# Kernel optimization log

Measured on AMD Instinct MI355X. Metric: run time of the kernel, lower is better.

The kernel has to match this reference:

```python
import jax, jax.numpy as jnp
import numpy as np

# CrossAttention (DFFNet): 1x1 convs produce q,k from depth and v from rgb;
# full dense attention over hw spatial tokens: softmax(q^T k) then v @ mask^T.

def setup_inputs() -> dict:
    key = jax.random.key(0)
    ks = jax.random.split(key, 8)
    B, C, H, W = 4, 256, 64, 64
    Cqk = C // 8  # ratio=8 -> 32
    s = 0.02
    return {
        "rgb":   jax.random.normal(ks[0], (B, C, H, W), jnp.float32),
        "depth": jax.random.normal(ks[1], (B, C, H, W), jnp.float32),
        "Wq": jax.random.normal(ks[2], (Cqk, C), jnp.float32) * s,
        "bq": jax.random.normal(ks[3], (Cqk,), jnp.float32) * s,
        "Wk": jax.random.normal(ks[4], (Cqk, C), jnp.float32) * s,
        "bk": jax.random.normal(ks[5], (Cqk,), jnp.float32) * s,
        "Wv": jax.random.normal(ks[6], (C, C), jnp.float32) * s,
        "bv": jax.random.normal(ks[7], (C,), jnp.float32) * s,
    }


def reference(rgb, depth, Wq, bq, Wk, bk, Wv, bv):
    B, C, H, W = rgb.shape
    hw = H * W
    d = depth.reshape(B, C, hw)   # [B, C, hw]
    r = rgb.reshape(B, C, hw)     # [B, C, hw]
    # 1x1 convs == channel-mixing linear maps
    q = jnp.einsum('oc,bcn->bon', Wq, d) + bq[None, :, None]  # [B, Cqk, hw]
    k = jnp.einsum('oc,bcn->bon', Wk, d) + bk[None, :, None]  # [B, Cqk, hw]
    v = jnp.einsum('oc,bcn->bon', Wv, r) + bv[None, :, None]  # [B, C, hw]
    # scores: q^T k -> [B, hw, hw], softmax over last dim
    scores = jnp.einsum('bcn,bcm->bnm', q, k)
    mask = jax.nn.softmax(scores, axis=-1)
    # feat = v @ mask^T  -> [B, C, hw]
    feat = jnp.einsum('bcm,bnm->bcn', v, mask)
    return feat.reshape(B, C, H, W)
```

## Files before the change

kernel.cpp:

```cpp
#include <hip/hip_runtime.h>
#include <stdint.h>

#define L2E 1.44269504088896340736f

typedef _Float16 half8 __attribute__((ext_vector_type(8)));
typedef float floatx4 __attribute__((ext_vector_type(4)));

static __device__ __forceinline__ unsigned short f32_to_f16u(float f) {
  union { _Float16 h; unsigned short s; } cv; cv.h = (_Float16)f; return cv.s;
}

__global__ __launch_bounds__(256) void proj_kernel(
    const float* __restrict__ rgb,
    const float* __restrict__ depth,
    const float* __restrict__ Wq, const float* __restrict__ bq,
    const float* __restrict__ Wk, const float* __restrict__ bk,
    const float* __restrict__ Wv, const float* __restrict__ bv,
    unsigned short* __restrict__ qT,
    unsigned short* __restrict__ kT,
    unsigned short* __restrict__ v)
{
  __shared__ __align__(16) unsigned short sW[64 * 256];

  const int n0 = blockIdx.x * 64;
  const int b  = blockIdx.y;
  const int z  = blockIdx.z;
  const int t  = threadIdx.x;
  const int w  = t >> 6;
  const int lane = t & 63;
  const int l15 = lane & 15;
  const int q4  = lane >> 4;

  const float* X = (z == 0) ? depth : rgb;
  const float* xb = X + (size_t)b * 256 * 4096;
  const int n_row = n0 + 16 * w + l15;
  const int colbase = (z == 0) ? 0 : (z - 1) * 64;

#pragma unroll
  for (int it = 0; it < 8; it++) {
    int L = it * 256 + t;
    int og = L >> 5;
    int phys = L & 31;
    int ci = phys ^ (og & 7);
    const float* wr;
    if (z == 0) wr = (og < 32) ? (Wq + (size_t)og * 256) : (Wk + (size_t)(og - 32) * 256);
    else        wr = Wv + (size_t)(colbase + og) * 256;
    float4 w0 = *(const float4*)(wr + ci * 8);
    float4 w1 = *(const float4*)(wr + ci * 8 + 4);
    half8 h;
    h[0] = (_Float16)w0.x; h[1] = (_Float16)w0.y; h[2] = (_Float16)w0.z; h[3] = (_Float16)w0.w;
    h[4] = (_Float16)w1.x; h[5] = (_Float16)w1.y; h[6] = (_Float16)w1.z; h[7] = (_Float16)w1.w;
    *(half8*)&sW[(size_t)L * 8] = h;
  }

  float bias[4];
#pragma unroll
  for (int ct = 0; ct < 4; ct++) {
    int og = ct * 16 + l15;
    if (z == 0) bias[ct] = (og < 32) ? bq[og] : bk[og - 32];
    else        bias[ct] = bv[colbase + og];
  }
  __syncthreads();

  floatx4 acc[4];
#pragma unroll
  for (int i = 0; i < 4; i++) acc[i] = (floatx4){0.f, 0.f, 0.f, 0.f};

#pragma unroll
  for (int ks = 0; ks < 8; ks++) {
    const int c0 = ks * 32;
    half8 a;
#pragma unroll
    for (int j = 0; j < 8; j++) {
      int c = c0 + q4 * 8 + j;
      a[j] = (_Float16)xb[(size_t)c * 4096 + n_row];
    }
    const int ci = ks * 4 + q4;
#pragma unroll
    for (int ct = 0; ct < 4; ct++) {
      int og = ct * 16 + l15;
      half8 bf = *(const half8*)&sW[og * 256 + ((ci ^ (og & 7)) * 8)];
      acc[ct] = __builtin_amdgcn_mfma_f32_16x16x32_f16(a, bf, acc[ct], 0, 0, 0);
    }
  }

  __syncthreads();

  if (z == 0) {
#pragma unroll
    for (int ct = 0; ct < 4; ct++) {
      int og = ct * 16 + l15;
#pragma unroll
      for (int r = 0; r < 4; r++) {
        int n = n0 + 16 * w + q4 * 4 + r;
        unsigned short hv = f32_to_f16u(acc[ct][r] + bias[ct]);
        if (og < 32) qT[((size_t)b * 4096 + n) * 32 + og] = hv;
        else         kT[((size_t)b * 4096 + n) * 32 + (og - 32)] = hv;
      }
    }
  } else {
    unsigned short* tile = sW;
#pragma unroll
    for (int ct = 0; ct < 4; ct++) {
#pragma unroll
      for (int r = 0; r < 4; r++) {
        int co_l = ct * 16 + l15;
        int nl = 16 * w + q4 * 4 + r;
        tile[co_l * 72 + nl] = f32_to_f16u(acc[ct][r] + bias[ct]);
      }
    }
    __syncthreads();
#pragma unroll
    for (int it = 0; it < 2; it++) {
      int co_l = it * 32 + (t >> 3);
      int ch = t & 7;
      int4 val = *(const int4*)&tile[co_l * 72 + ch * 8];
      *(int4*)&v[((size_t)b * 256 + colbase + co_l) * 4096 + n0 + ch * 8] = val;
    }
  }
}

__global__ __launch_bounds__(256, 4) void attn_kernel(
    const unsigned short* __restrict__ qT,
    const unsigned short* __restrict__ kT,
    const unsigned short* __restrict__ v,
    unsigned short* __restrict__ Op,
    float* __restrict__ lW)
{
  __shared__ __align__(16) unsigned char smem[36864];
  unsigned short* sV = (unsigned short*)smem;
  unsigned short* sK = (unsigned short*)(smem + 16384);
  unsigned short* sP = (unsigned short*)(smem + 18432);

  const int n0 = blockIdx.x * 64;
  const int b  = blockIdx.y;
  const int chunk = blockIdx.z;
  const int t  = threadIdx.x;
  const int w  = t >> 6;
  const int lane = t & 63;
  const int l15 = lane & 15;
  const int q4  = lane >> 4;

  const unsigned short* qrow = qT + ((size_t)b * 4096 + n0 + 16 * w + l15) * 32 + q4 * 8;
  half8 aq = *(const half8*)qrow;

  const unsigned short* vB = v  + (size_t)b * 256 * 4096;
  const unsigned short* kB = kT + (size_t)b * 4096 * 32;
  unsigned short* sPw = sP + w * 640;

  float lsum[4] = {0.f, 0.f, 0.f, 0.f};
  floatx4 acc[16];
#pragma unroll
  for (int ct = 0; ct < 16; ct++) acc[ct] = (floatx4){0.f, 0.f, 0.f, 0.f};
  const floatx4 zf = (floatx4){0.f, 0.f, 0.f, 0.f};

  const int mbase = chunk * 1024;
  for (int mi = 0; mi < 1024; mi += 32) {
    const int m0 = mbase + mi;
    __syncthreads();
#pragma unroll
    for (int j = 0; j < 4; j++) {
      int lin = j * 256 + t;
      int c = lin >> 2;
      int p = lin & 3;
      int lc = p ^ ((c >> 1) & 3);
      uint4 val = *(const uint4*)&vB[(size_t)c * 4096 + m0 + lc * 8];
      *(uint4*)&sV[lin * 8] = val;
    }
    if (t < 128) {
      int m = t >> 2, p = t & 3, lc = p ^ ((m >> 1) & 3);
      uint4 val = *(const uint4*)&kB[(size_t)(m0 + m) * 32 + lc * 8];
      *(uint4*)&sK[t * 8] = val;
    }
    __syncthreads();

    half8 bk0 = *(const half8*)&sK[l15 * 32 + ((q4 ^ ((l15 >> 1) & 3)) * 8)];
    half8 bk1 = *(const half8*)&sK[(16 + l15) * 32 + ((q4 ^ (((16 + l15) >> 1) & 3)) * 8)];
    floatx4 s0 = __builtin_amdgcn_mfma_f32_16x16x32_f16(aq, bk0, zf, 0, 0, 0);
    floatx4 s1 = __builtin_amdgcn_mfma_f32_16x16x32_f16(aq, bk1, zf, 0, 0, 0);

    float p0[4], p1[4];
#pragma unroll
    for (int r = 0; r < 4; r++) {
      p0[r] = exp2f(s0[r] * L2E);
      p1[r] = exp2f(s1[r] * L2E);
      lsum[r] += p0[r] + p1[r];
    }
#pragma unroll
    for (int r = 0; r < 4; r++) {
      int row = q4 * 4 + r;
      sPw[row * 40 + l15]      = f32_to_f16u(p0[r]);
      sPw[row * 40 + 16 + l15] = f32_to_f16u(p1[r]);
    }
    asm volatile("s_waitcnt lgkmcnt(0)" ::: "memory");
    half8 ap = *(const half8*)&sPw[l15 * 40 + q4 * 8];
#pragma unroll
    for (int ct = 0; ct < 16; ct++) {
      int co = ct * 16 + l15;
      half8 bv8 = *(const half8*)&sV[co * 32 + ((q4 ^ ((co >> 1) & 3)) * 8)];
      acc[ct] = __builtin_amdgcn_mfma_f32_16x16x32_f16(ap, bv8, acc[ct], 0, 0, 0);
    }
  }

#pragma unroll
  for (int off = 1; off < 16; off <<= 1) {
#pragma unroll
    for (int r = 0; r < 4; r++) lsum[r] += __shfl_xor(lsum[r], off);
  }
  if (l15 == 0) {
#pragma unroll
    for (int r = 0; r < 4; r++)
      lW[((size_t)chunk * 4 + b) * 4096 + n0 + 16 * w + q4 * 4 + r] = lsum[r];
  }

  unsigned short* sO = (unsigned short*)smem;
#pragma unroll
  for (int pass = 0; pass < 2; pass++) {
    __syncthreads();
#pragma unroll
    for (int cl = 0; cl < 8; cl++) {
      int ct = pass * 8 + cl;
      int co_l = cl * 16 + l15;
#pragma unroll
      for (int r = 0; r < 4; r++) {
        int nl = 16 * w + q4 * 4 + r;
        sO[co_l * 72 + nl] = f32_to_f16u(acc[ct][r]);
      }
    }
    __syncthreads();
#pragma unroll
    for (int s = 0; s < 4; s++) {
      int co_l = s * 32 + (t >> 3);
      int ch = t & 7;
      int4 val = *(const int4*)&sO[co_l * 72 + ch * 8];
      *(int4*)&Op[(((size_t)chunk * 4 + b) * 256 + pass * 128 + co_l) * 4096 + n0 + ch * 8] = val;
    }
  }
}

__global__ __launch_bounds__(256) void combine_kernel(
    const unsigned short* __restrict__ Op,
    const float* __restrict__ lW,
    float* __restrict__ out)
{
  const int t = threadIdx.x;
  const int b = blockIdx.y;
  const size_t n8 = (size_t)blockIdx.x * 2048 + (size_t)t * 8;
  const int co0 = blockIdx.z * 8;

  float sum[8] = {0.f, 0.f, 0.f, 0.f, 0.f, 0.f, 0.f, 0.f};
#pragma unroll
  for (int ch = 0; ch < 4; ch++) {
    const float* lp = lW + ((size_t)ch * 4 + b) * 4096 + n8;
    float4 a0 = *(const float4*)lp;
    float4 a1 = *(const float4*)(lp + 4);
    sum[0] += a0.x; sum[1] += a0.y; sum[2] += a0.z; sum[3] += a0.w;
    sum[4] += a1.x; sum[5] += a1.y; sum[6] += a1.z; sum[7] += a1.w;
  }
  float rl[8];
#pragma unroll
  for (int i = 0; i < 8; i++) rl[i] = 1.0f / sum[i];

#pragma unroll
  for (int cc = 0; cc < 8; cc++) {
    int co = co0 + cc;
    float o[8] = {0.f, 0.f, 0.f, 0.f, 0.f, 0.f, 0.f, 0.f};
#pragma unroll
    for (int ch = 0; ch < 4; ch++) {
      half8 hv = *(const half8*)&Op[(((size_t)ch * 4 + b) * 256 + co) * 4096 + n8];
#pragma unroll
      for (int i = 0; i < 8; i++) o[i] += (float)hv[i];
    }
    float* op = out + ((size_t)b * 256 + co) * 4096 + n8;
    float4 r0, r1;
    r0.x = o[0] * rl[0]; r0.y = o[1] * rl[1]; r0.z = o[2] * rl[2]; r0.w = o[3] * rl[3];
    r1.x = o[4] * rl[4]; r1.y = o[5] * rl[5]; r1.z = o[6] * rl[6]; r1.w = o[7] * rl[7];
    *(float4*)op = r0;
    *(float4*)(op + 4) = r1;
  }
}

extern "C" void kernel_launch(void* const* d_in, const int* in_sizes, int n_in,
                              void* d_out, int out_size, void* d_ws, size_t ws_size,
                              hipStream_t stream) {
  const float* rgb   = (const float*)d_in[0];
  const float* depth = (const float*)d_in[1];
  const float* Wq    = (const float*)d_in[2];
  const float* bq    = (const float*)d_in[3];
  const float* Wk    = (const float*)d_in[4];
  const float* bk    = (const float*)d_in[5];
  const float* Wv    = (const float*)d_in[6];
  const float* bv    = (const float*)d_in[7];
  float* out = (float*)d_out;

  unsigned short* qT = (unsigned short*)d_ws;
  unsigned short* kT = qT + (size_t)4 * 4096 * 32;
  unsigned short* vW = kT + (size_t)4 * 4096 * 32;
  unsigned short* Op = vW + (size_t)4 * 256 * 4096;
  float* lW = (float*)(Op + (size_t)4 * 4 * 256 * 4096);

  dim3 pg(64, 4, 5);
  proj_kernel<<<pg, 256, 0, stream>>>(rgb, depth, Wq, bq, Wk, bk, Wv, bv, qT, kT, vW);
  dim3 ag(64, 4, 4);
  attn_kernel<<<ag, 256, 0, stream>>>(qT, kT, vW, Op, lW);
  dim3 cg(2, 4, 32);
  combine_kernel<<<cg, 256, 0, stream>>>(Op, lW, out);
}
```

Baseline: 172.0 us.

## Split attention channels across blocks and use 32x32 MFMA for PV

The attention kernel now splits the 256 output channels into two halves across blocks, doubling the grid. It switches the P·V product to 32x32x16 MFMA tiles with P shared through LDS by all waves, and loads K directly from global into registers instead of staging it in LDS. Smaller LDS and accumulator footprints allow higher occupancy hints, at the cost of recomputing QK scores and exponentials twice per query tile and adding an extra barrier per iteration. The projection kernel prefetches the next input slice into registers, and the combine kernel is flattened to one channel per block.

Result: slower. 196.5 us (+14.2%).

```diff
diff --git a/kernel.cpp b/kernel.cpp
--- a/kernel.cpp
+++ b/kernel.cpp
@@ -5,12 +5,14 @@
 
 typedef _Float16 half8 __attribute__((ext_vector_type(8)));
 typedef float floatx4 __attribute__((ext_vector_type(4)));
+typedef float floatx16 __attribute__((ext_vector_type(16)));
 
 static __device__ __forceinline__ unsigned short f32_to_f16u(float f) {
   union { _Float16 h; unsigned short s; } cv; cv.h = (_Float16)f; return cv.s;
 }
-
-__global__ __launch_bounds__(256) void proj_kernel(
+static __device__ __forceinline__ _Float16 f32h(float f) { return (_Float16)f; }
+
+__global__ __launch_bounds__(256, 5) void proj_kernel(
     const float* __restrict__ rgb,
     const float* __restrict__ depth,
     const float* __restrict__ Wq, const float* __restrict__ bq,
@@ -30,10 +32,11 @@
   const int lane = t & 63;
   const int l15 = lane & 15;
   const int q4  = lane >> 4;
+  const int n_row = n0 + 16 * w + l15;
 
   const float* X = (z == 0) ? depth : rgb;
   const float* xb = X + (size_t)b * 256 * 4096;
-  const int n_row = n0 + 16 * w + l15;
+  const float* xrow = xb + n_row;
   const int colbase = (z == 0) ? 0 : (z - 1) * 64;
 
 #pragma unroll
@@ -48,8 +51,8 @@
     float4 w0 = *(const float4*)(wr + ci * 8);
     float4 w1 = *(const float4*)(wr + ci * 8 + 4);
     half8 h;
-    h[0] = (_Float16)w0.x; h[1] = (_Float16)w0.y; h[2] = (_Float16)w0.z; h[3] = (_Float16)w0.w;
-    h[4] = (_Float16)w1.x; h[5] = (_Float16)w1.y; h[6] = (_Float16)w1.z; h[7] = (_Float16)w1.w;
+    h[0] = f32h(w0.x); h[1] = f32h(w0.y); h[2] = f32h(w0.z); h[3] = f32h(w0.w);
+    h[4] = f32h(w1.x); h[5] = f32h(w1.y); h[6] = f32h(w1.z); h[7] = f32h(w1.w);
     *(half8*)&sW[(size_t)L * 8] = h;
   }
 
@@ -66,14 +69,19 @@
 #pragma unroll
   for (int i = 0; i < 4; i++) acc[i] = (floatx4){0.f, 0.f, 0.f, 0.f};
 
+  float af[8];
+#pragma unroll
+  for (int j = 0; j < 8; j++) af[j] = xrow[(size_t)(q4 * 8 + j) * 4096];
+
 #pragma unroll
   for (int ks = 0; ks < 8; ks++) {
-    const int c0 = ks * 32;
     half8 a;
 #pragma unroll
-    for (int j = 0; j < 8; j++) {
-      int c = c0 + q4 * 8 + j;
-      a[j] = (_Float16)xb[(size_t)c * 4096 + n_row];
+    for (int j = 0; j < 8; j++) a[j] = (_Float16)af[j];
+    if (ks < 7) {
+#pragma unroll
+      for (int j = 0; j < 8; j++)
+        af[j] = xrow[(size_t)(ks * 32 + 32 + q4 * 8 + j) * 4096];
     }
     const int ci = ks * 4 + q4;
 #pragma unroll
@@ -120,46 +128,53 @@
   }
 }
 
-__global__ __launch_bounds__(256, 4) void attn_kernel(
+__global__ __launch_bounds__(256, 6) void attn_kernel(
     const unsigned short* __restrict__ qT,
     const unsigned short* __restrict__ kT,
     const unsigned short* __restrict__ v,
     unsigned short* __restrict__ Op,
     float* __restrict__ lW)
 {
-  __shared__ __align__(16) unsigned char smem[36864];
+  __shared__ __align__(16) unsigned char smem[18432];
   unsigned short* sV = (unsigned short*)smem;
-  unsigned short* sK = (unsigned short*)(smem + 16384);
-  unsigned short* sP = (unsigned short*)(smem + 18432);
+  unsigned short* sP = (unsigned short*)(smem + 8192);
 
   const int n0 = blockIdx.x * 64;
   const int b  = blockIdx.y;
-  const int chunk = blockIdx.z;
+  const int chunk = blockIdx.z >> 1;
+  const int half  = blockIdx.z & 1;
   const int t  = threadIdx.x;
   const int w  = t >> 6;
   const int lane = t & 63;
   const int l15 = lane & 15;
   const int q4  = lane >> 4;
+  const int l31 = lane & 31;
+  const int hi  = lane >> 5;
+  const int co0 = half * 128;
 
   const unsigned short* qrow = qT + ((size_t)b * 4096 + n0 + 16 * w + l15) * 32 + q4 * 8;
   half8 aq = *(const half8*)qrow;
 
-  const unsigned short* vB = v  + (size_t)b * 256 * 4096;
+  const unsigned short* vB = v  + (size_t)b * 256 * 4096 + (size_t)co0 * 4096;
   const unsigned short* kB = kT + (size_t)b * 4096 * 32;
-  unsigned short* sPw = sP + w * 640;
 
   float lsum[4] = {0.f, 0.f, 0.f, 0.f};
-  floatx4 acc[16];
-#pragma unroll
-  for (int ct = 0; ct < 16; ct++) acc[ct] = (floatx4){0.f, 0.f, 0.f, 0.f};
+  floatx16 acc[2];
+#pragma unroll
+  for (int nt = 0; nt < 2; nt++)
+#pragma unroll
+    for (int i = 0; i < 16; i++) acc[nt][i] = 0.f;
   const floatx4 zf = (floatx4){0.f, 0.f, 0.f, 0.f};
 
   const int mbase = chunk * 1024;
   for (int mi = 0; mi < 1024; mi += 32) {
     const int m0 = mbase + mi;
+    half8 bk0 = *(const half8*)&kB[(size_t)(m0 + l15) * 32 + q4 * 8];
+    half8 bk1 = *(const half8*)&kB[(size_t)(m0 + 16 + l15) * 32 + q4 * 8];
+
     __syncthreads();
 #pragma unroll
-    for (int j = 0; j < 4; j++) {
+    for (int j = 0; j < 2; j++) {
       int lin = j * 256 + t;
       int c = lin >> 2;
       int p = lin & 3;
@@ -167,15 +182,8 @@
       uint4 val = *(const uint4*)&vB[(size_t)c * 4096 + m0 + lc * 8];
       *(uint4*)&sV[lin * 8] = val;
     }
-    if (t < 128) {
-      int m = t >> 2, p = t & 3, lc = p ^ ((m >> 1) & 3);
-      uint4 val = *(const uint4*)&kB[(size_t)(m0 + m) * 32 + lc * 8];
-      *(uint4*)&sK[t * 8] = val;
-    }
     __syncthreads();
 
-    half8 bk0 = *(const half8*)&sK[l15 * 32 + ((q4 ^ ((l15 >> 1) & 3)) * 8)];
-    half8 bk1 = *(const half8*)&sK[(16 + l15) * 32 + ((q4 ^ (((16 + l15) >> 1) & 3)) * 8)];
     floatx4 s0 = __builtin_amdgcn_mfma_f32_16x16x32_f16(aq, bk0, zf, 0, 0, 0);
     floatx4 s1 = __builtin_amdgcn_mfma_f32_16x16x32_f16(aq, bk1, zf, 0, 0, 0);
 
@@ -188,17 +196,22 @@
     }
 #pragma unroll
     for (int r = 0; r < 4; r++) {
-      int row = q4 * 4 + r;
-      sPw[row * 40 + l15]      = f32_to_f16u(p0[r]);
-      sPw[row * 40 + 16 + l15] = f32_to_f16u(p1[r]);
-    }
-    asm volatile("s_waitcnt lgkmcnt(0)" ::: "memory");
-    half8 ap = *(const half8*)&sPw[l15 * 40 + q4 * 8];
-#pragma unroll
-    for (int ct = 0; ct < 16; ct++) {
-      int co = ct * 16 + l15;
-      half8 bv8 = *(const half8*)&sV[co * 32 + ((q4 ^ ((co >> 1) & 3)) * 8)];
-      acc[ct] = __builtin_amdgcn_mfma_f32_16x16x32_f16(ap, bv8, acc[ct], 0, 0, 0);
+      int row = w * 16 + q4 * 4 + r;
+      sP[row * 40 + l15]      = f32_to_f16u(p0[r]);
+      sP[row * 40 + 16 + l15] = f32_to_f16u(p1[r]);
+    }
+    __syncthreads();
+
+    const int c_lw = w * 32 + l31;
+#pragma unroll
+    for (int kst = 0; kst < 2; kst++) {
+      int lc = (kst * 2 + hi) ^ ((c_lw >> 1) & 3);
+      half8 bvv = *(const half8*)&sV[(c_lw * 4 + lc) * 8];
+#pragma unroll
+      for (int nt = 0; nt < 2; nt++) {
+        half8 ap = *(const half8*)&sP[(nt * 32 + l31) * 40 + kst * 16 + hi * 8];
+        acc[nt] = __builtin_amdgcn_mfma_f32_32x32x16_f16(ap, bvv, acc[nt], 0, 0, 0);
+      }
     }
   }
 
@@ -207,34 +220,35 @@
 #pragma unroll
     for (int r = 0; r < 4; r++) lsum[r] += __shfl_xor(lsum[r], off);
   }
-  if (l15 == 0) {
+  if (half == 0 && l15 == 0) {
 #pragma unroll
     for (int r = 0; r < 4; r++)
       lW[((size_t)chunk * 4 + b) * 4096 + n0 + 16 * w + q4 * 4 + r] = lsum[r];
   }
 
+  __syncthreads();
   unsigned short* sO = (unsigned short*)smem;
-#pragma unroll
-  for (int pass = 0; pass < 2; pass++) {
-    __syncthreads();
-#pragma unroll
-    for (int cl = 0; cl < 8; cl++) {
-      int ct = pass * 8 + cl;
-      int co_l = cl * 16 + l15;
-#pragma unroll
-      for (int r = 0; r < 4; r++) {
-        int nl = 16 * w + q4 * 4 + r;
-        sO[co_l * 72 + nl] = f32_to_f16u(acc[ct][r]);
-      }
-    }
-    __syncthreads();
-#pragma unroll
-    for (int s = 0; s < 4; s++) {
-      int co_l = s * 32 + (t >> 3);
-      int ch = t & 7;
-      int4 val = *(const int4*)&sO[co_l * 72 + ch * 8];
-      *(int4*)&Op[(((size_t)chunk * 4 + b) * 256 + pass * 128 + co_l) * 4096 + n0 + ch * 8] = val;
-    }
+  const int co_l = w * 32 + l31;
+#pragma unroll
+  for (int nt = 0; nt < 2; nt++) {
+#pragma unroll
+    for (int g = 0; g < 4; g++) {
+      int nl = nt * 32 + g * 8 + hi * 4;
+      ushort4 pk;
+      pk.x = f32_to_f16u(acc[nt][g * 4 + 0]);
+      pk.y = f32_to_f16u(acc[nt][g * 4 + 1]);
+      pk.z = f32_to_f16u(acc[nt][g * 4 + 2]);
+      pk.w = f32_to_f16u(acc[nt][g * 4 + 3]);
+      *(ushort4*)&sO[co_l * 72 + nl] = pk;
+    }
+  }
+  __syncthreads();
+#pragma unroll
+  for (int s = 0; s < 4; s++) {
+    int cl = s * 32 + (t >> 3);
+    int ch = t & 7;
+    int4 val = *(const int4*)&sO[cl * 72 + ch * 8];
+    *(int4*)&Op[(((size_t)chunk * 4 + b) * 256 + co0 + cl) * 4096 + n0 + ch * 8] = val;
   }
 }
 
@@ -245,10 +259,11 @@
 {
   const int t = threadIdx.x;
   const int b = blockIdx.y;
+  const int co = blockIdx.z;
   const size_t n8 = (size_t)blockIdx.x * 2048 + (size_t)t * 8;
-  const int co0 = blockIdx.z * 8;
 
   float sum[8] = {0.f, 0.f, 0.f, 0.f, 0.f, 0.f, 0.f, 0.f};
+  float o[8]   = {0.f, 0.f, 0.f, 0.f, 0.f, 0.f, 0.f, 0.f};
 #pragma unroll
   for (int ch = 0; ch < 4; ch++) {
     const float* lp = lW + ((size_t)ch * 4 + b) * 4096 + n8;
@@ -256,28 +271,16 @@
     float4 a1 = *(const float4*)(lp + 4);
     sum[0] += a0.x; sum[1] += a0.y; sum[2] += a0.z; sum[3] += a0.w;
     sum[4] += a1.x; sum[5] += a1.y; sum[6] += a1.z; sum[7] += a1.w;
-  }
-  float rl[8];
-#pragma unroll
-  for (int i = 0; i < 8; i++) rl[i] = 1.0f / sum[i];
-
-#pragma unroll
-  for (int cc = 0; cc < 8; cc++) {
-    int co = co0 + cc;
-    float o[8] = {0.f, 0.f, 0.f, 0.f, 0.f, 0.f, 0.f, 0.f};
-#pragma unroll
-    for (int ch = 0; ch < 4; ch++) {
-      half8 hv = *(const half8*)&Op[(((size_t)ch * 4 + b) * 256 + co) * 4096 + n8];
-#pragma unroll
-      for (int i = 0; i < 8; i++) o[i] += (float)hv[i];
-    }
-    float* op = out + ((size_t)b * 256 + co) * 4096 + n8;
-    float4 r0, r1;
-    r0.x = o[0] * rl[0]; r0.y = o[1] * rl[1]; r0.z = o[2] * rl[2]; r0.w = o[3] * rl[3];
-    r1.x = o[4] * rl[4]; r1.y = o[5] * rl[5]; r1.z = o[6] * rl[6]; r1.w = o[7] * rl[7];
-    *(float4*)op = r0;
-    *(float4*)(op + 4) = r1;
-  }
+    half8 hv = *(const half8*)&Op[(((size_t)ch * 4 + b) * 256 + co) * 4096 + n8];
+#pragma unroll
+    for (int i = 0; i < 8; i++) o[i] += (float)hv[i];
+  }
+  float* op = out + ((size_t)b * 256 + co) * 4096 + n8;
+  float4 r0, r1;
+  r0.x = o[0] / sum[0]; r0.y = o[1] / sum[1]; r0.z = o[2] / sum[2]; r0.w = o[3] / sum[3];
+  r1.x = o[4] / sum[4]; r1.y = o[5] / sum[5]; r1.z = o[6] / sum[6]; r1.w = o[7] / sum[7];
+  *(float4*)op = r0;
+  *(float4*)(op + 4) = r1;
 }
 
 extern "C" void kernel_launch(void* const* d_in, const int* in_sizes, int n_in,
@@ -301,8 +304,8 @@
 
   dim3 pg(64, 4, 5);
   proj_kernel<<<pg, 256, 0, stream>>>(rgb, depth, Wq, bq, Wk, bk, Wv, bv, qT, kT, vW);
-  dim3 ag(64, 4, 4);
+  dim3 ag(64, 4, 8);
   attn_kernel<<<ag, 256, 0, stream>>>(qT, kT, vW, Op, lW);
-  dim3 cg(2, 4, 32);
+  dim3 cg(2, 4, 256);
   combine_kernel<<<cg, 256, 0, stream>>>(Op, lW, out);
 }
```
